# Optimization experiments

Hardware: AMD Instinct MI355X
Metric: run time of the kernel (lower is better)

Reference implementation:

```python
import jax, jax.numpy as jnp
import numpy as np

D_MODEL = 1024
N_HEADS = 16
HEAD_DIM = D_MODEL // N_HEADS
D_FF = 4096
BATCH = 128
MEM_LEN = 1024
LN_EPS = 1e-5


def _layernorm(x, gamma, beta):
    mu = jnp.mean(x, axis=-1, keepdims=True)
    var = jnp.mean(jnp.square(x - mu), axis=-1, keepdims=True)
    return (x - mu) * jax.lax.rsqrt(var + LN_EPS) * gamma + beta


def setup_inputs() -> dict:
    key = jax.random.key(0)
    ks = jax.random.split(key, 12)
    s = 0.02
    return {
        "x": jax.random.normal(ks[0], (BATCH, D_MODEL), jnp.float32),
        "memory_keys": jax.random.normal(ks[1], (BATCH, MEM_LEN, D_MODEL), jnp.float32),
        "memory_values": jax.random.normal(ks[2], (BATCH, MEM_LEN, D_MODEL), jnp.float32),
        "alibi_bias": jax.random.normal(ks[3], (N_HEADS, 1, MEM_LEN), jnp.float32),
        "Wq": jax.random.normal(ks[4], (D_MODEL, D_MODEL), jnp.float32) * s,
        "bq": jnp.zeros((D_MODEL,), jnp.float32),
        "Wo": jax.random.normal(ks[5], (D_MODEL, D_MODEL), jnp.float32) * s,
        "bo": jnp.zeros((D_MODEL,), jnp.float32),
        "W1": jax.random.normal(ks[6], (D_MODEL, D_FF), jnp.float32) * s,
        "b1": jnp.zeros((D_FF,), jnp.float32),
        "W2": jax.random.normal(ks[7], (D_FF, D_MODEL), jnp.float32) * s,
        "b2": jnp.zeros((D_MODEL,), jnp.float32),
        "g1": jnp.ones((D_MODEL,), jnp.float32),
        "be1": jnp.zeros((D_MODEL,), jnp.float32),
        "g2": jnp.ones((D_MODEL,), jnp.float32),
        "be2": jnp.zeros((D_MODEL,), jnp.float32),
    }


def reference(x, memory_keys, memory_values, alibi_bias,
              Wq, bq, Wo, bo, W1, b1, W2, b2, g1, be1, g2, be2):
    B = x.shape[0]
    M = memory_keys.shape[1]
    # Q projection for the single query position: (B, H, hd)
    q = (x @ Wq + bq).reshape(B, N_HEADS, HEAD_DIM)
    k = memory_keys.reshape(B, M, N_HEADS, HEAD_DIM)
    v = memory_values.reshape(B, M, N_HEADS, HEAD_DIM)
    scale = 1.0 / np.sqrt(HEAD_DIM).astype(np.float32)
    # scores: (B, H, M) = q . k + ALiBi bias (broadcast over batch)
    scores = jnp.einsum("bhd,bmhd->bhm", q, k) * scale + alibi_bias[:, 0, :][None]
    attn = jax.nn.softmax(scores, axis=-1)
    attn_out = jnp.einsum("bhm,bmhd->bhd", attn, v).reshape(B, D_MODEL)
    attn_out = attn_out @ Wo + bo
    # residual + norm1 (dropout disabled in eval mode)
    h = _layernorm(x + attn_out, g1, be1)
    ff = jax.nn.relu(h @ W1 + b1) @ W2 + b2
    return _layernorm(h + ff, g2, be2)
```

## Files before the change

kernel.cpp:

```cpp
#include <hip/hip_runtime.h>
#include <hip/hip_bf16.h>
#include <math.h>

#define BATCH   128
#define DMODEL  1024
#define NHEADS  16
#define HEADDIM 64
#define DFF     4096
#define MEMLEN  1024
#define SPLIT   8
#define CHUNK   (MEMLEN / SPLIT)

typedef __attribute__((ext_vector_type(8))) __bf16 bf16x8;
typedef __attribute__((ext_vector_type(4))) float  f32x4;

template<int ACT>
__global__ __launch_bounds__(256) void gemm_bf16_k(
    const float* __restrict__ A, const float* __restrict__ W,
    const float* __restrict__ bias, float* __restrict__ C,
    int M, int N, int K)
{
    const int t    = threadIdx.x;
    const int lane = t & 63;
    const int w    = t >> 6;
    const int n0   = blockIdx.x * 64;
    const int m0   = blockIdx.y * 64;

    __shared__ __bf16 As[64 * 56];
    __shared__ __bf16 Bs[64 * 56];

    f32x4 acc[4] = {f32x4{0,0,0,0}, f32x4{0,0,0,0}, f32x4{0,0,0,0}, f32x4{0,0,0,0}};

    const int ar = t >> 2;
    const int ac = (t & 3) * 8;
    const int bn = t & 63;
    const int bk = (t >> 6) * 8;

    const int q   = lane >> 4;
    const int l15 = lane & 15;

    for (int k0 = 0; k0 < K; k0 += 32) {
        {
            const float* ap = A + (size_t)(m0 + ar) * K + k0 + ac;
            float4 a01 = *(const float4*)ap;
            float4 a23 = *(const float4*)(ap + 4);
            bf16x8 av;
            av[0] = (__bf16)a01.x; av[1] = (__bf16)a01.y;
            av[2] = (__bf16)a01.z; av[3] = (__bf16)a01.w;
            av[4] = (__bf16)a23.x; av[5] = (__bf16)a23.y;
            av[6] = (__bf16)a23.z; av[7] = (__bf16)a23.w;
            *(bf16x8*)&As[ar * 56 + ac] = av;
        }
        {
            const float* wp = W + (size_t)(k0 + bk) * N + n0 + bn;
            bf16x8 bv;
            #pragma unroll
            for (int j = 0; j < 8; j++) bv[j] = (__bf16)wp[(size_t)j * N];
            *(bf16x8*)&Bs[bn * 56 + bk] = bv;
        }
        __syncthreads();
        bf16x8 af = *(const bf16x8*)&As[(w * 16 + l15) * 56 + q * 8];
        #pragma unroll
        for (int c = 0; c < 4; c++) {
            bf16x8 bfv = *(const bf16x8*)&Bs[(c * 16 + l15) * 56 + q * 8];
            acc[c] = __builtin_amdgcn_mfma_f32_16x16x32_bf16(af, bfv, acc[c], 0, 0, 0);
        }
        __syncthreads();
    }

    #pragma unroll
    for (int c = 0; c < 4; c++) {
        const int col = n0 + c * 16 + l15;
        const float bb = bias[col];
        #pragma unroll
        for (int r = 0; r < 4; r++) {
            const int row = m0 + w * 16 + q * 4 + r;
            float v = acc[c][r] + bb;
            if (ACT) v = fmaxf(v, 0.0f);
            C[(size_t)row * N + col] = v;
        }
    }
}

__global__ __launch_bounds__(256) void attn_partial_k(
    const float* __restrict__ q, const float* __restrict__ Kd,
    const float* __restrict__ Vd, const float* __restrict__ alibi,
    float* __restrict__ pacc, float* __restrict__ pm, float* __restrict__ pl)
{
    const int s = blockIdx.x;
    const int b = blockIdx.y;
    const int t = threadIdx.x;
    const int h = t >> 4;

    const float scale = 0.125f;
    float4 qv = *(const float4*)&q[(size_t)b * DMODEL + 4 * t];
    qv.x *= scale; qv.y *= scale; qv.z *= scale; qv.w *= scale;

    float mrun = -INFINITY;
    float lrun = 0.0f;
    float4 acc = {0.f, 0.f, 0.f, 0.f};

    const size_t base = (size_t)b * MEMLEN * DMODEL + 4 * t;
    const float* __restrict__ ali = alibi + (size_t)h * MEMLEN;

    const int mEnd = s * CHUNK + CHUNK;
    for (int m = s * CHUNK; m < mEnd; m++) {
        const size_t off = base + (size_t)m * DMODEL;
        const float4 kv = *(const float4*)&Kd[off];
        float d = kv.x * qv.x + kv.y * qv.y + kv.z * qv.z + kv.w * qv.w;
        d += __shfl_xor(d, 1);
        d += __shfl_xor(d, 2);
        d += __shfl_xor(d, 4);
        d += __shfl_xor(d, 8);
        const float sc = d + ali[m];
        const float nm = fmaxf(mrun, sc);
        const float alpha = __expf(mrun - nm);
        const float p = __expf(sc - nm);
        lrun = lrun * alpha + p;
        const float4 vv = *(const float4*)&Vd[off];
        acc.x = acc.x * alpha + p * vv.x;
        acc.y = acc.y * alpha + p * vv.y;
        acc.z = acc.z * alpha + p * vv.z;
        acc.w = acc.w * alpha + p * vv.w;
        mrun = nm;
    }

    *(float4*)&pacc[((size_t)(b * SPLIT + s)) * DMODEL + 4 * t] = acc;
    if ((t & 15) == 0) {
        pm[(b * SPLIT + s) * NHEADS + h] = mrun;
        pl[(b * SPLIT + s) * NHEADS + h] = lrun;
    }
}

__global__ __launch_bounds__(256) void attn_combine_k(
    const float* __restrict__ pacc, const float* __restrict__ pm,
    const float* __restrict__ pl, float* __restrict__ attn_out)
{
    const int b = blockIdx.x;
    const int t = threadIdx.x;
    const int h = t >> 4;

    float M = -INFINITY;
    #pragma unroll
    for (int s = 0; s < SPLIT; s++)
        M = fmaxf(M, pm[(b * SPLIT + s) * NHEADS + h]);

    float L = 0.0f;
    float4 acc = {0.f, 0.f, 0.f, 0.f};
    #pragma unroll
    for (int s = 0; s < SPLIT; s++) {
        const float wgt = __expf(pm[(b * SPLIT + s) * NHEADS + h] - M);
        L += pl[(b * SPLIT + s) * NHEADS + h] * wgt;
        const float4 pa = *(const float4*)&pacc[((size_t)(b * SPLIT + s)) * DMODEL + 4 * t];
        acc.x += pa.x * wgt; acc.y += pa.y * wgt;
        acc.z += pa.z * wgt; acc.w += pa.w * wgt;
    }
    const float inv = 1.0f / L;
    float4 o = {acc.x * inv, acc.y * inv, acc.z * inv, acc.w * inv};
    *(float4*)&attn_out[(size_t)b * DMODEL + 4 * t] = o;
}

__global__ __launch_bounds__(256) void ln_k(
    const float* __restrict__ x, const float* __restrict__ y,
    const float* __restrict__ g, const float* __restrict__ be,
    float* __restrict__ out)
{
    const int b = blockIdx.x;
    const int t = threadIdx.x;
    const float4 xv = *(const float4*)&x[(size_t)b * DMODEL + 4 * t];
    const float4 yv = *(const float4*)&y[(size_t)b * DMODEL + 4 * t];
    float4 sv = {xv.x + yv.x, xv.y + yv.y, xv.z + yv.z, xv.w + yv.w};

    float sum = sv.x + sv.y + sv.z + sv.w;
    float sq  = sv.x * sv.x + sv.y * sv.y + sv.z * sv.z + sv.w * sv.w;
    #pragma unroll
    for (int mask = 1; mask < 64; mask <<= 1) {
        sum += __shfl_xor(sum, mask);
        sq  += __shfl_xor(sq, mask);
    }
    __shared__ float red[8];
    const int w = t >> 6;
    if ((t & 63) == 0) { red[w * 2] = sum; red[w * 2 + 1] = sq; }
    __syncthreads();
    sum = red[0] + red[2] + red[4] + red[6];
    sq  = red[1] + red[3] + red[5] + red[7];

    const float mu  = sum * (1.0f / DMODEL);
    const float var = sq * (1.0f / DMODEL) - mu * mu;
    const float rs  = rsqrtf(var + 1e-5f);

    const float4 gv  = *(const float4*)&g[4 * t];
    const float4 bev = *(const float4*)&be[4 * t];
    float4 o;
    o.x = (sv.x - mu) * rs * gv.x + bev.x;
    o.y = (sv.y - mu) * rs * gv.y + bev.y;
    o.z = (sv.z - mu) * rs * gv.z + bev.z;
    o.w = (sv.w - mu) * rs * gv.w + bev.w;
    *(float4*)&out[(size_t)b * DMODEL + 4 * t] = o;
}

extern "C" void kernel_launch(void* const* d_in, const int* in_sizes, int n_in,
                              void* d_out, int out_size, void* d_ws, size_t ws_size,
                              hipStream_t stream)
{
    const float* x   = (const float*)d_in[0];
    const float* mk  = (const float*)d_in[1];
    const float* mv  = (const float*)d_in[2];
    const float* ab  = (const float*)d_in[3];
    const float* Wq  = (const float*)d_in[4];
    const float* bq  = (const float*)d_in[5];
    const float* Wo  = (const float*)d_in[6];
    const float* bo  = (const float*)d_in[7];
    const float* W1  = (const float*)d_in[8];
    const float* b1  = (const float*)d_in[9];
    const float* W2  = (const float*)d_in[10];
    const float* b2  = (const float*)d_in[11];
    const float* g1  = (const float*)d_in[12];
    const float* be1 = (const float*)d_in[13];
    const float* g2  = (const float*)d_in[14];
    const float* be2 = (const float*)d_in[15];
    float* out = (float*)d_out;

    float* wsf  = (float*)d_ws;
    float* qbuf = wsf;
    float* attn = wsf + 131072;
    float* tmp  = wsf + 262144;
    float* hbuf = wsf + 393216;
    float* tmp2 = wsf + 524288;
    float* ffb  = wsf + 655360;
    float* pacc = wsf + 1179648;
    float* pm   = wsf + 2228224;
    float* pl   = wsf + 2244608;

    gemm_bf16_k<0><<<dim3(DMODEL / 64, BATCH / 64), 256, 0, stream>>>(
        x, Wq, bq, qbuf, BATCH, DMODEL, DMODEL);
    attn_partial_k<<<dim3(SPLIT, BATCH), 256, 0, stream>>>(
        qbuf, mk, mv, ab, pacc, pm, pl);
    attn_combine_k<<<BATCH, 256, 0, stream>>>(pacc, pm, pl, attn);
    gemm_bf16_k<0><<<dim3(DMODEL / 64, BATCH / 64), 256, 0, stream>>>(
        attn, Wo, bo, tmp, BATCH, DMODEL, DMODEL);
    ln_k<<<BATCH, 256, 0, stream>>>(x, tmp, g1, be1, hbuf);
    gemm_bf16_k<1><<<dim3(DFF / 64, BATCH / 64), 256, 0, stream>>>(
        hbuf, W1, b1, ffb, BATCH, DFF, DMODEL);
    gemm_bf16_k<0><<<dim3(DMODEL / 64, BATCH / 64), 256, 0, stream>>>(
        ffb, W2, b2, tmp2, BATCH, DMODEL, DFF);
    ln_k<<<BATCH, 256, 0, stream>>>(hbuf, tmp2, g2, be2, out);
}
```

Before: 1.217 ms.

## Fuse whole layer into one persistent cooperative kernel with split-K GEMMs

Replaces the eight separate launches with a single cooperative persistent kernel whose phases are separated by grid-wide syncs. The GEMMs become split-K with double-buffered LDS tiles, and intermediate activations are stored in bf16 so later GEMMs load them directly. The attention split doubles to 16 chunks and drops the running-max softmax in favour of plain exp sums, which removes the rescaling work but can overflow for large scores. The change also needs a much larger workspace and adds grid-sync overhead between phases.

```diff
diff --git a/kernel.cpp b/kernel.cpp
--- a/kernel.cpp
+++ b/kernel.cpp
@@ -1,6 +1,9 @@
 #include <hip/hip_runtime.h>
 #include <hip/hip_bf16.h>
+#include <hip/hip_cooperative_groups.h>
 #include <math.h>
+
+namespace cg = cooperative_groups;
 
 #define BATCH   128
 #define DMODEL  1024
@@ -8,241 +11,349 @@
 #define HEADDIM 64
 #define DFF     4096
 #define MEMLEN  1024
-#define SPLIT   8
+#define SPLIT   16
 #define CHUNK   (MEMLEN / SPLIT)
+#define QSPLIT  8
+#define F1SPLIT 4
+#define F2SPLIT 16
 
 typedef __attribute__((ext_vector_type(8))) __bf16 bf16x8;
+typedef __attribute__((ext_vector_type(4))) __bf16 bf16x4;
 typedef __attribute__((ext_vector_type(4))) float  f32x4;
 
-template<int ACT>
-__global__ __launch_bounds__(256) void gemm_bf16_k(
-    const float* __restrict__ A, const float* __restrict__ W,
-    const float* __restrict__ bias, float* __restrict__ C,
-    int M, int N, int K)
+struct Params {
+    const float *x, *mk, *mv, *ab;
+    const float *Wq, *bq, *Wo, *bo, *W1, *b1, *W2, *b2, *g1, *be1, *g2, *be2;
+    float* out;
+    float *qpart, *qsum, *tmppart, *hbuf, *ffbpart, *tmp2part, *pacc, *pl;
+    __bf16 *attnb, *hbf, *ff1act;
+};
+
+template<int ABF16, int NXLOG2, int KCHUNK>
+__device__ __forceinline__ void gemm_phase(
+    const float* __restrict__ Af, const __bf16* __restrict__ Ab,
+    const float* __restrict__ W, const float* __restrict__ bias,
+    float* __restrict__ C, int N, int K, int J, int NB,
+    __bf16 (&As)[2][64 * 56], __bf16 (&Bs)[2][64 * 56])
 {
     const int t    = threadIdx.x;
     const int lane = t & 63;
     const int w    = t >> 6;
-    const int n0   = blockIdx.x * 64;
-    const int m0   = blockIdx.y * 64;
-
-    __shared__ __bf16 As[64 * 56];
-    __shared__ __bf16 Bs[64 * 56];
-
-    f32x4 acc[4] = {f32x4{0,0,0,0}, f32x4{0,0,0,0}, f32x4{0,0,0,0}, f32x4{0,0,0,0}};
-
-    const int ar = t >> 2;
-    const int ac = (t & 3) * 8;
-    const int bn = t & 63;
-    const int bk = (t >> 6) * 8;
-
-    const int q   = lane >> 4;
-    const int l15 = lane & 15;
-
-    for (int k0 = 0; k0 < K; k0 += 32) {
+    const int ar = t >> 2, ac = (t & 3) * 8;
+    const int bn = t & 63, bk = w * 8;
+    const int q = lane >> 4, l15 = lane & 15;
+    constexpr int ITERS = KCHUNK / 32;
+
+    for (int job = blockIdx.x; job < J; job += NB) {
+        const int nxi  = job & ((1 << NXLOG2) - 1);
+        const int rest = job >> NXLOG2;
+        const int my   = rest & 1;
+        const int z    = rest >> 1;
+        const int n0 = nxi * 64, m0 = my * 64, kbeg = z * KCHUNK;
+
+        __syncthreads();
+
+        f32x4 acc[4] = {f32x4{0,0,0,0}, f32x4{0,0,0,0}, f32x4{0,0,0,0}, f32x4{0,0,0,0}};
+
+        const float* wB   = W + (size_t)(kbeg + bk) * N + n0 + bn;
+        const size_t aOff = (size_t)(m0 + ar) * K + kbeg + ac;
+
         {
-            const float* ap = A + (size_t)(m0 + ar) * K + k0 + ac;
-            float4 a01 = *(const float4*)ap;
-            float4 a23 = *(const float4*)(ap + 4);
             bf16x8 av;
-            av[0] = (__bf16)a01.x; av[1] = (__bf16)a01.y;
-            av[2] = (__bf16)a01.z; av[3] = (__bf16)a01.w;
-            av[4] = (__bf16)a23.x; av[5] = (__bf16)a23.y;
-            av[6] = (__bf16)a23.z; av[7] = (__bf16)a23.w;
-            *(bf16x8*)&As[ar * 56 + ac] = av;
-        }
+            if constexpr (ABF16) {
+                av = *(const bf16x8*)(Ab + aOff);
+            } else {
+                const float* ap = Af + aOff;
+                float4 a0 = *(const float4*)ap, a1 = *(const float4*)(ap + 4);
+                av[0]=(__bf16)a0.x; av[1]=(__bf16)a0.y; av[2]=(__bf16)a0.z; av[3]=(__bf16)a0.w;
+                av[4]=(__bf16)a1.x; av[5]=(__bf16)a1.y; av[6]=(__bf16)a1.z; av[7]=(__bf16)a1.w;
+            }
+            bf16x8 bv;
+            #pragma unroll
+            for (int j = 0; j < 8; j++) bv[j] = (__bf16)wB[(size_t)j * N];
+            *(bf16x8*)&As[0][ar * 56 + ac] = av;
+            *(bf16x8*)&Bs[0][bn * 56 + bk] = bv;
+        }
+        __syncthreads();
+
+        int cur = 0;
+        #pragma unroll
+        for (int it = 1; it < ITERS; ++it) {
+            bf16x8 avn;
+            float ax[8];
+            if constexpr (ABF16) {
+                avn = *(const bf16x8*)(Ab + aOff + it * 32);
+            } else {
+                const float* ap = Af + aOff + it * 32;
+                float4 a0 = *(const float4*)ap, a1 = *(const float4*)(ap + 4);
+                ax[0]=a0.x; ax[1]=a0.y; ax[2]=a0.z; ax[3]=a0.w;
+                ax[4]=a1.x; ax[5]=a1.y; ax[6]=a1.z; ax[7]=a1.w;
+            }
+            float br[8];
+            const float* wp = wB + (size_t)(it * 32) * N;
+            #pragma unroll
+            for (int j = 0; j < 8; j++) br[j] = wp[(size_t)j * N];
+
+            bf16x8 af = *(const bf16x8*)&As[cur][(w * 16 + l15) * 56 + q * 8];
+            #pragma unroll
+            for (int c = 0; c < 4; c++) {
+                bf16x8 bfv = *(const bf16x8*)&Bs[cur][(c * 16 + l15) * 56 + q * 8];
+                acc[c] = __builtin_amdgcn_mfma_f32_16x16x32_bf16(af, bfv, acc[c], 0, 0, 0);
+            }
+
+            if constexpr (!ABF16) {
+                #pragma unroll
+                for (int j = 0; j < 8; j++) avn[j] = (__bf16)ax[j];
+            }
+            bf16x8 bvn;
+            #pragma unroll
+            for (int j = 0; j < 8; j++) bvn[j] = (__bf16)br[j];
+            *(bf16x8*)&As[cur ^ 1][ar * 56 + ac] = avn;
+            *(bf16x8*)&Bs[cur ^ 1][bn * 56 + bk] = bvn;
+            __syncthreads();
+            cur ^= 1;
+        }
+
         {
-            const float* wp = W + (size_t)(k0 + bk) * N + n0 + bn;
-            bf16x8 bv;
-            #pragma unroll
-            for (int j = 0; j < 8; j++) bv[j] = (__bf16)wp[(size_t)j * N];
-            *(bf16x8*)&Bs[bn * 56 + bk] = bv;
+            bf16x8 af = *(const bf16x8*)&As[cur][(w * 16 + l15) * 56 + q * 8];
+            #pragma unroll
+            for (int c = 0; c < 4; c++) {
+                bf16x8 bfv = *(const bf16x8*)&Bs[cur][(c * 16 + l15) * 56 + q * 8];
+                acc[c] = __builtin_amdgcn_mfma_f32_16x16x32_bf16(af, bfv, acc[c], 0, 0, 0);
+            }
+        }
+
+        float* Cp = C + (size_t)z * ((size_t)BATCH * N);
+        #pragma unroll
+        for (int c = 0; c < 4; c++) {
+            const int col = n0 + c * 16 + l15;
+            const float bb = (z == 0) ? bias[col] : 0.0f;
+            #pragma unroll
+            for (int r = 0; r < 4; r++) {
+                const int row = m0 + w * 16 + q * 4 + r;
+                Cp[(size_t)row * N + col] = acc[c][r] + bb;
+            }
+        }
+    }
+}
+
+template<int NPARTS, bool WRITE_BF16>
+__device__ __forceinline__ void ln_phase(
+    const float* __restrict__ xres, const float* __restrict__ parts,
+    const float* __restrict__ g, const float* __restrict__ be,
+    float* __restrict__ of32, __bf16* __restrict__ obf,
+    int NB, float (&red)[8])
+{
+    const int t = threadIdx.x;
+    for (int b = blockIdx.x; b < BATCH; b += NB) {
+        float4 sv = *(const float4*)&xres[(size_t)b * DMODEL + 4 * t];
+        #pragma unroll
+        for (int z = 0; z < NPARTS; z++) {
+            const float4 yv = *(const float4*)
+                &parts[(size_t)z * (BATCH * DMODEL) + (size_t)b * DMODEL + 4 * t];
+            sv.x += yv.x; sv.y += yv.y; sv.z += yv.z; sv.w += yv.w;
+        }
+        float sum = sv.x + sv.y + sv.z + sv.w;
+        float sq  = sv.x * sv.x + sv.y * sv.y + sv.z * sv.z + sv.w * sv.w;
+        #pragma unroll
+        for (int mask = 1; mask < 64; mask <<= 1) {
+            sum += __shfl_xor(sum, mask);
+            sq  += __shfl_xor(sq, mask);
         }
         __syncthreads();
-        bf16x8 af = *(const bf16x8*)&As[(w * 16 + l15) * 56 + q * 8];
-        #pragma unroll
-        for (int c = 0; c < 4; c++) {
-            bf16x8 bfv = *(const bf16x8*)&Bs[(c * 16 + l15) * 56 + q * 8];
-            acc[c] = __builtin_amdgcn_mfma_f32_16x16x32_bf16(af, bfv, acc[c], 0, 0, 0);
-        }
+        if ((t & 63) == 0) { red[(t >> 6) * 2] = sum; red[(t >> 6) * 2 + 1] = sq; }
         __syncthreads();
-    }
-
-    #pragma unroll
-    for (int c = 0; c < 4; c++) {
-        const int col = n0 + c * 16 + l15;
-        const float bb = bias[col];
-        #pragma unroll
-        for (int r = 0; r < 4; r++) {
-            const int row = m0 + w * 16 + q * 4 + r;
-            float v = acc[c][r] + bb;
-            if (ACT) v = fmaxf(v, 0.0f);
-            C[(size_t)row * N + col] = v;
+        sum = red[0] + red[2] + red[4] + red[6];
+        sq  = red[1] + red[3] + red[5] + red[7];
+
+        const float mu  = sum * (1.0f / DMODEL);
+        const float var = sq * (1.0f / DMODEL) - mu * mu;
+        const float rs  = rsqrtf(var + 1e-5f);
+
+        const float4 gv  = *(const float4*)&g[4 * t];
+        const float4 bev = *(const float4*)&be[4 * t];
+        float4 o;
+        o.x = (sv.x - mu) * rs * gv.x + bev.x;
+        o.y = (sv.y - mu) * rs * gv.y + bev.y;
+        o.z = (sv.z - mu) * rs * gv.z + bev.z;
+        o.w = (sv.w - mu) * rs * gv.w + bev.w;
+        *(float4*)&of32[(size_t)b * DMODEL + 4 * t] = o;
+        if constexpr (WRITE_BF16) {
+            bf16x4 ob;
+            ob[0] = (__bf16)o.x; ob[1] = (__bf16)o.y;
+            ob[2] = (__bf16)o.z; ob[3] = (__bf16)o.w;
+            *(bf16x4*)&obf[(size_t)b * DMODEL + 4 * t] = ob;
         }
     }
 }
 
-__global__ __launch_bounds__(256) void attn_partial_k(
-    const float* __restrict__ q, const float* __restrict__ Kd,
-    const float* __restrict__ Vd, const float* __restrict__ alibi,
-    float* __restrict__ pacc, float* __restrict__ pm, float* __restrict__ pl)
+__global__ __launch_bounds__(256) void fused_k(Params p)
 {
-    const int s = blockIdx.x;
-    const int b = blockIdx.y;
-    const int t = threadIdx.x;
-    const int h = t >> 4;
-
-    const float scale = 0.125f;
-    float4 qv = *(const float4*)&q[(size_t)b * DMODEL + 4 * t];
-    qv.x *= scale; qv.y *= scale; qv.z *= scale; qv.w *= scale;
-
-    float mrun = -INFINITY;
-    float lrun = 0.0f;
-    float4 acc = {0.f, 0.f, 0.f, 0.f};
-
-    const size_t base = (size_t)b * MEMLEN * DMODEL + 4 * t;
-    const float* __restrict__ ali = alibi + (size_t)h * MEMLEN;
-
-    const int mEnd = s * CHUNK + CHUNK;
-    for (int m = s * CHUNK; m < mEnd; m++) {
-        const size_t off = base + (size_t)m * DMODEL;
-        const float4 kv = *(const float4*)&Kd[off];
-        float d = kv.x * qv.x + kv.y * qv.y + kv.z * qv.z + kv.w * qv.w;
-        d += __shfl_xor(d, 1);
-        d += __shfl_xor(d, 2);
-        d += __shfl_xor(d, 4);
-        d += __shfl_xor(d, 8);
-        const float sc = d + ali[m];
-        const float nm = fmaxf(mrun, sc);
-        const float alpha = __expf(mrun - nm);
-        const float p = __expf(sc - nm);
-        lrun = lrun * alpha + p;
-        const float4 vv = *(const float4*)&Vd[off];
-        acc.x = acc.x * alpha + p * vv.x;
-        acc.y = acc.y * alpha + p * vv.y;
-        acc.z = acc.z * alpha + p * vv.z;
-        acc.w = acc.w * alpha + p * vv.w;
-        mrun = nm;
-    }
-
-    *(float4*)&pacc[((size_t)(b * SPLIT + s)) * DMODEL + 4 * t] = acc;
-    if ((t & 15) == 0) {
-        pm[(b * SPLIT + s) * NHEADS + h] = mrun;
-        pl[(b * SPLIT + s) * NHEADS + h] = lrun;
-    }
-}
-
-__global__ __launch_bounds__(256) void attn_combine_k(
-    const float* __restrict__ pacc, const float* __restrict__ pm,
-    const float* __restrict__ pl, float* __restrict__ attn_out)
-{
-    const int b = blockIdx.x;
-    const int t = threadIdx.x;
-    const int h = t >> 4;
-
-    float M = -INFINITY;
-    #pragma unroll
-    for (int s = 0; s < SPLIT; s++)
-        M = fmaxf(M, pm[(b * SPLIT + s) * NHEADS + h]);
-
-    float L = 0.0f;
-    float4 acc = {0.f, 0.f, 0.f, 0.f};
-    #pragma unroll
-    for (int s = 0; s < SPLIT; s++) {
-        const float wgt = __expf(pm[(b * SPLIT + s) * NHEADS + h] - M);
-        L += pl[(b * SPLIT + s) * NHEADS + h] * wgt;
-        const float4 pa = *(const float4*)&pacc[((size_t)(b * SPLIT + s)) * DMODEL + 4 * t];
-        acc.x += pa.x * wgt; acc.y += pa.y * wgt;
-        acc.z += pa.z * wgt; acc.w += pa.w * wgt;
-    }
-    const float inv = 1.0f / L;
-    float4 o = {acc.x * inv, acc.y * inv, acc.z * inv, acc.w * inv};
-    *(float4*)&attn_out[(size_t)b * DMODEL + 4 * t] = o;
-}
-
-__global__ __launch_bounds__(256) void ln_k(
-    const float* __restrict__ x, const float* __restrict__ y,
-    const float* __restrict__ g, const float* __restrict__ be,
-    float* __restrict__ out)
-{
-    const int b = blockIdx.x;
-    const int t = threadIdx.x;
-    const float4 xv = *(const float4*)&x[(size_t)b * DMODEL + 4 * t];
-    const float4 yv = *(const float4*)&y[(size_t)b * DMODEL + 4 * t];
-    float4 sv = {xv.x + yv.x, xv.y + yv.y, xv.z + yv.z, xv.w + yv.w};
-
-    float sum = sv.x + sv.y + sv.z + sv.w;
-    float sq  = sv.x * sv.x + sv.y * sv.y + sv.z * sv.z + sv.w * sv.w;
-    #pragma unroll
-    for (int mask = 1; mask < 64; mask <<= 1) {
-        sum += __shfl_xor(sum, mask);
-        sq  += __shfl_xor(sq, mask);
-    }
-    __shared__ float red[8];
-    const int w = t >> 6;
-    if ((t & 63) == 0) { red[w * 2] = sum; red[w * 2 + 1] = sq; }
-    __syncthreads();
-    sum = red[0] + red[2] + red[4] + red[6];
-    sq  = red[1] + red[3] + red[5] + red[7];
-
-    const float mu  = sum * (1.0f / DMODEL);
-    const float var = sq * (1.0f / DMODEL) - mu * mu;
-    const float rs  = rsqrtf(var + 1e-5f);
-
-    const float4 gv  = *(const float4*)&g[4 * t];
-    const float4 bev = *(const float4*)&be[4 * t];
-    float4 o;
-    o.x = (sv.x - mu) * rs * gv.x + bev.x;
-    o.y = (sv.y - mu) * rs * gv.y + bev.y;
-    o.z = (sv.z - mu) * rs * gv.z + bev.z;
-    o.w = (sv.w - mu) * rs * gv.w + bev.w;
-    *(float4*)&out[(size_t)b * DMODEL + 4 * t] = o;
+    __shared__ __bf16 As[2][64 * 56];
+    __shared__ __bf16 Bs[2][64 * 56];
+    __shared__ float  red[8];
+
+    cg::grid_group grid = cg::this_grid();
+    const int NB = gridDim.x;
+    const int t  = threadIdx.x;
+
+    gemm_phase<0, 4, DMODEL / QSPLIT>(p.x, nullptr, p.Wq, p.bq, p.qpart,
+                                      DMODEL, DMODEL, 16 * 2 * QSPLIT, NB, As, Bs);
+    grid.sync();
+
+    for (int b = blockIdx.x; b < BATCH; b += NB) {
+        const size_t idx = (size_t)b * DMODEL + 4 * t;
+        float4 a = {0.f, 0.f, 0.f, 0.f};
+        #pragma unroll
+        for (int z = 0; z < QSPLIT; z++) {
+            const float4 v = *(const float4*)&p.qpart[(size_t)z * (BATCH * DMODEL) + idx];
+            a.x += v.x; a.y += v.y; a.z += v.z; a.w += v.w;
+        }
+        a.x *= 0.125f; a.y *= 0.125f; a.z *= 0.125f; a.w *= 0.125f;
+        *(float4*)&p.qsum[idx] = a;
+    }
+    grid.sync();
+
+    for (int job = blockIdx.x; job < SPLIT * BATCH; job += NB) {
+        const int s = job & (SPLIT - 1);
+        const int b = job >> 4;
+        const int h = t >> 4;
+
+        const float4 qv = *(const float4*)&p.qsum[(size_t)b * DMODEL + 4 * t];
+        float  l   = 0.0f;
+        f32x4  acc = {0.f, 0.f, 0.f, 0.f};
+
+        const size_t base = (size_t)b * MEMLEN * DMODEL + 4 * t;
+        const float* __restrict__ ali = p.ab + (size_t)h * MEMLEN + s * CHUNK;
+        const size_t off0 = base + (size_t)(s * CHUNK) * DMODEL;
+
+        #pragma unroll 4
+        for (int i = 0; i < CHUNK; i++) {
+            const size_t off = off0 + (size_t)i * DMODEL;
+            const float4 kv = *(const float4*)&p.mk[off];
+            const float4 vv = *(const float4*)&p.mv[off];
+            float d = kv.x * qv.x + kv.y * qv.y + kv.z * qv.z + kv.w * qv.w;
+            d += __shfl_xor(d, 1);
+            d += __shfl_xor(d, 2);
+            d += __shfl_xor(d, 4);
+            d += __shfl_xor(d, 8);
+            const float pw = __expf(d + ali[i]);
+            l += pw;
+            acc.x += pw * vv.x;
+            acc.y += pw * vv.y;
+            acc.z += pw * vv.z;
+            acc.w += pw * vv.w;
+        }
+        *(f32x4*)&p.pacc[((size_t)(b * SPLIT + s)) * DMODEL + 4 * t] = acc;
+        if ((t & 15) == 0) p.pl[(b * SPLIT + s) * NHEADS + h] = l;
+    }
+    grid.sync();
+
+    for (int b = blockIdx.x; b < BATCH; b += NB) {
+        const int h = t >> 4;
+        float  L   = 0.0f;
+        float4 acc = {0.f, 0.f, 0.f, 0.f};
+        #pragma unroll 4
+        for (int s = 0; s < SPLIT; s++) {
+            L += p.pl[(b * SPLIT + s) * NHEADS + h];
+            const float4 pa = *(const float4*)
+                &p.pacc[((size_t)(b * SPLIT + s)) * DMODEL + 4 * t];
+            acc.x += pa.x; acc.y += pa.y; acc.z += pa.z; acc.w += pa.w;
+        }
+        const float inv = 1.0f / L;
+        bf16x4 o;
+        o[0] = (__bf16)(acc.x * inv); o[1] = (__bf16)(acc.y * inv);
+        o[2] = (__bf16)(acc.z * inv); o[3] = (__bf16)(acc.w * inv);
+        *(bf16x4*)&p.attnb[(size_t)b * DMODEL + 4 * t] = o;
+    }
+    grid.sync();
+
+    gemm_phase<1, 4, DMODEL / QSPLIT>(nullptr, p.attnb, p.Wo, p.bo, p.tmppart,
+                                      DMODEL, DMODEL, 16 * 2 * QSPLIT, NB, As, Bs);
+    grid.sync();
+
+    ln_phase<QSPLIT, true>(p.x, p.tmppart, p.g1, p.be1, p.hbuf, p.hbf, NB, red);
+    grid.sync();
+
+    gemm_phase<1, 6, DMODEL / F1SPLIT>(nullptr, p.hbf, p.W1, p.b1, p.ffbpart,
+                                       DFF, DMODEL, 64 * 2 * F1SPLIT, NB, As, Bs);
+    grid.sync();
+
+    for (int job = blockIdx.x; job < (BATCH * DFF) / 2048; job += NB) {
+        const size_t base = (size_t)job * 2048 + t * 8;
+        float4 s0 = {0.f, 0.f, 0.f, 0.f}, s1 = {0.f, 0.f, 0.f, 0.f};
+        #pragma unroll
+        for (int z = 0; z < F1SPLIT; z++) {
+            const float* pp = p.ffbpart + (size_t)z * ((size_t)BATCH * DFF) + base;
+            const float4 a = *(const float4*)pp;
+            const float4 b4 = *(const float4*)(pp + 4);
+            s0.x += a.x;  s0.y += a.y;  s0.z += a.z;  s0.w += a.w;
+            s1.x += b4.x; s1.y += b4.y; s1.z += b4.z; s1.w += b4.w;
+        }
+        bf16x8 o;
+        o[0] = (__bf16)fmaxf(s0.x, 0.f); o[1] = (__bf16)fmaxf(s0.y, 0.f);
+        o[2] = (__bf16)fmaxf(s0.z, 0.f); o[3] = (__bf16)fmaxf(s0.w, 0.f);
+        o[4] = (__bf16)fmaxf(s1.x, 0.f); o[5] = (__bf16)fmaxf(s1.y, 0.f);
+        o[6] = (__bf16)fmaxf(s1.z, 0.f); o[7] = (__bf16)fmaxf(s1.w, 0.f);
+        *(bf16x8*)&p.ff1act[base] = o;
+    }
+    grid.sync();
+
+    gemm_phase<1, 4, DFF / F2SPLIT>(nullptr, p.ff1act, p.W2, p.b2, p.tmp2part,
+                                    DMODEL, DFF, 16 * 2 * F2SPLIT, NB, As, Bs);
+    grid.sync();
+
+    ln_phase<F2SPLIT, false>(p.hbuf, p.tmp2part, p.g2, p.be2, p.out, nullptr, NB, red);
 }
 
 extern "C" void kernel_launch(void* const* d_in, const int* in_sizes, int n_in,
                               void* d_out, int out_size, void* d_ws, size_t ws_size,
                               hipStream_t stream)
 {
-    const float* x   = (const float*)d_in[0];
-    const float* mk  = (const float*)d_in[1];
-    const float* mv  = (const float*)d_in[2];
-    const float* ab  = (const float*)d_in[3];
-    const float* Wq  = (const float*)d_in[4];
-    const float* bq  = (const float*)d_in[5];
-    const float* Wo  = (const float*)d_in[6];
-    const float* bo  = (const float*)d_in[7];
-    const float* W1  = (const float*)d_in[8];
-    const float* b1  = (const float*)d_in[9];
-    const float* W2  = (const float*)d_in[10];
-    const float* b2  = (const float*)d_in[11];
-    const float* g1  = (const float*)d_in[12];
-    const float* be1 = (const float*)d_in[13];
-    const float* g2  = (const float*)d_in[14];
-    const float* be2 = (const float*)d_in[15];
-    float* out = (float*)d_out;
-
-    float* wsf  = (float*)d_ws;
-    float* qbuf = wsf;
-    float* attn = wsf + 131072;
-    float* tmp  = wsf + 262144;
-    float* hbuf = wsf + 393216;
-    float* tmp2 = wsf + 524288;
-    float* ffb  = wsf + 655360;
-    float* pacc = wsf + 1179648;
-    float* pm   = wsf + 2228224;
-    float* pl   = wsf + 2244608;
-
-    gemm_bf16_k<0><<<dim3(DMODEL / 64, BATCH / 64), 256, 0, stream>>>(
-        x, Wq, bq, qbuf, BATCH, DMODEL, DMODEL);
-    attn_partial_k<<<dim3(SPLIT, BATCH), 256, 0, stream>>>(
-        qbuf, mk, mv, ab, pacc, pm, pl);
-    attn_combine_k<<<BATCH, 256, 0, stream>>>(pacc, pm, pl, attn);
-    gemm_bf16_k<0><<<dim3(DMODEL / 64, BATCH / 64), 256, 0, stream>>>(
-        attn, Wo, bo, tmp, BATCH, DMODEL, DMODEL);
-    ln_k<<<BATCH, 256, 0, stream>>>(x, tmp, g1, be1, hbuf);
-    gemm_bf16_k<1><<<dim3(DFF / 64, BATCH / 64), 256, 0, stream>>>(
-        hbuf, W1, b1, ffb, BATCH, DFF, DMODEL);
-    gemm_bf16_k<0><<<dim3(DMODEL / 64, BATCH / 64), 256, 0, stream>>>(
-        ffb, W2, b2, tmp2, BATCH, DMODEL, DFF);
-    ln_k<<<BATCH, 256, 0, stream>>>(hbuf, tmp2, g2, be2, out);
+    float* wsf = (float*)d_ws;
+
+    Params P;
+    P.x   = (const float*)d_in[0];
+    P.mk  = (const float*)d_in[1];
+    P.mv  = (const float*)d_in[2];
+    P.ab  = (const float*)d_in[3];
+    P.Wq  = (const float*)d_in[4];
+    P.bq  = (const float*)d_in[5];
+    P.Wo  = (const float*)d_in[6];
+    P.bo  = (const float*)d_in[7];
+    P.W1  = (const float*)d_in[8];
+    P.b1  = (const float*)d_in[9];
+    P.W2  = (const float*)d_in[10];
+    P.b2  = (const float*)d_in[11];
+    P.g1  = (const float*)d_in[12];
+    P.be1 = (const float*)d_in[13];
+    P.g2  = (const float*)d_in[14];
+    P.be2 = (const float*)d_in[15];
+    P.out = (float*)d_out;
+
+    P.qpart    = wsf;
+    P.qsum     = wsf + 1048576;
+    P.tmppart  = wsf + 1179648;
+    P.hbuf     = wsf + 2228224;
+    P.ffbpart  = wsf + 2359296;
+    P.tmp2part = wsf + 4456448;
+    P.pacc     = wsf + 6553600;
+    P.pl       = wsf + 8650752;
+    P.attnb    = (__bf16*)(wsf + 8683520);
+    P.hbf      = (__bf16*)(wsf + 8749056);
+    P.ff1act   = (__bf16*)(wsf + 8814592);
+
+    static int NB = 0;
+    if (NB == 0) {
+        int per = 0;
+        if (hipOccupancyMaxActiveBlocksPerMultiprocessor(
+                &per, (const void*)fused_k, 256, 0) != hipSuccess || per < 1)
+            per = 2;
+        NB = per * 256;
+        if (NB > 2048) NB = 2048;
+    }
+
+    void* args[] = { (void*)&P };
+    hipLaunchCooperativeKernel((const void*)fused_k, dim3(NB), dim3(256),
+                               args, 0, stream);
 }
```

After: 1.357 ms. 1.11x slower.
